# Kernel optimization log

Hardware: AMD Instinct MI355X
Metric: run time of the kernel (lower is better)

## Reference

```python
import jax, jax.numpy as jnp
import numpy as np

B, N, E, D, L, NC = 64, 128, 1024, 256, 2, 7
BETA = 0.3  # args.diffloss
BIG = 1e30  # mask_logic constant (score - (1-adj)*1e30), as in torch source lineage


def setup_inputs():
    key = jax.random.key(0)
    ks = iter(jax.random.split(key, 48))
    def p(shape, s=0.02):
        return jax.random.normal(next(ks), shape, jnp.float32) * s
    inp = {}
    inp["features"] = jax.random.normal(next(ks), (B, N, E), jnp.float32)
    inp["adj_1"] = jax.random.randint(next(ks), (B, N, N), 0, 2, jnp.int32)
    inp["adj_2"] = jax.random.randint(next(ks), (B, N, N), 0, 2, jnp.int32)
    inp["s_mask"] = jax.random.randint(next(ks), (B, N, N), 0, 2, jnp.int32)
    inp["s_mask_onehot"] = jnp.zeros((B, N, N, 2), jnp.int32)
    inp["lengths"] = jnp.full((B,), N, jnp.int32)
    inp["fc1_w"] = p((D, E)); inp["fc1_b"] = jnp.zeros((D,), jnp.float32)
    # GRUCell params (torch layout: weight_ih (3D,D) order r,z,n)
    for nm in ["gcs", "gps", "gcl", "gpl"]:
        inp[nm + "_wih"] = p((L, 3 * D, D)); inp[nm + "_whh"] = p((L, 3 * D, D))
        inp[nm + "_bih"] = jnp.zeros((L, 3 * D), jnp.float32)
        inp[nm + "_bhh"] = jnp.zeros((L, 3 * D), jnp.float32)
    # GatDot params per layer: linear1 (Q proj), linear2 (K proj)
    for nm in ["gats", "gatl"]:
        inp[nm + "_wq"] = p((L, D, D)); inp[nm + "_bq"] = jnp.zeros((L, D), jnp.float32)
        inp[nm + "_wk"] = p((L, D, D)); inp[nm + "_bk"] = jnp.zeros((L, D), jnp.float32)
    inp["affine1"] = p((2 * D, 2 * D), 0.05)
    inp["affine2"] = p((2 * D, 2 * D), 0.05)
    IN = 4 * D + E  # hidden*2*2 + emb_dim
    inp["mlp_w1"] = p((D, IN)); inp["mlp_b1"] = jnp.zeros((D,), jnp.float32)
    inp["mlp_w2"] = p((D, D)); inp["mlp_b2"] = jnp.zeros((D,), jnp.float32)
    inp["out_w"] = p((NC, D)); inp["out_b"] = jnp.zeros((NC,), jnp.float32)
    return inp


def gru_cell(x, h, wih, whh, bih, bhh):
    gi = x @ wih.T + bih
    gh = h @ whh.T + bhh
    ir, iz, in_ = jnp.split(gi, 3, axis=-1)
    hr, hz, hn = jnp.split(gh, 3, axis=-1)
    r = jax.nn.sigmoid(ir + hr)
    z = jax.nn.sigmoid(iz + hz)
    n = jnp.tanh(in_ + r * hn)
    return (1.0 - z) * n + z * h


def dag_pass(H_in, adj, gat, cpar, ppar):
    """Sequential DAG pass: per-utterance masked dot-product gather + GRU-C/GRU-P."""
    wq, bq, wk, bk = gat
    n = H_in.shape[1]
    idx = jnp.arange(n)

    def step(carry, inp):
        H1, Kb = carry            # H1: [B,N,D] written prefix; Kb = linear2(H1)
        i, x, arow = inp          # x: [B,D], arow: [B,N]
        q = x @ wq.T + bq
        scores = jnp.einsum('bnd,bd->bn', Kb, q)
        # torch: alpha - (1-adj)*1e30 over prefix :i; positions >= i excluded
        logits = scores - (1.0 - arow) * BIG - (idx >= i).astype(scores.dtype) * (2.0 * BIG)
        w = jax.nn.softmax(logits, axis=-1)
        M = jnp.einsum('bn,bnd->bd', w, H1)  # exactly 0 at i==0 (buffer zeros)
        C = gru_cell(x, M, *cpar)   # grus_c(input=x, hidden=M)
        P = gru_cell(M, x, *ppar)   # grus_p(input=M, hidden=x)
        h = C + P
        H1 = jax.lax.dynamic_update_slice(H1, h[:, None, :], (0, i, 0))
        Kb = jax.lax.dynamic_update_slice(Kb, (h @ wk.T + bk)[:, None, :], (0, i, 0))
        return (H1, Kb), None

    init = (jnp.zeros_like(H_in), jnp.zeros_like(H_in))
    xs = (idx, jnp.swapaxes(H_in, 0, 1), jnp.swapaxes(adj, 0, 1))
    (H1, _), _ = jax.lax.scan(step, init, xs)
    return H1


def diff_loss_fn(a, b):
    # orthogonality (DSN-style) loss between short/long channel features
    x = a.reshape(-1, a.shape[-1])
    y = b.reshape(-1, b.shape[-1])
    x = x - x.mean(axis=0, keepdims=True)
    y = y - y.mean(axis=0, keepdims=True)
    x = x / (jnp.linalg.norm(x, axis=1, keepdims=True) + 1e-6)
    y = y / (jnp.linalg.norm(y, axis=1, keepdims=True) + 1e-6)
    return jnp.mean((x.T @ y) ** 2)


def _forward(features, adj_1, adj_2,
             fc1_w, fc1_b,
             gcs_wih, gcs_whh, gcs_bih, gcs_bhh,
             gps_wih, gps_whh, gps_bih, gps_bhh,
             gcl_wih, gcl_whh, gcl_bih, gcl_bhh,
             gpl_wih, gpl_whh, gpl_bih, gpl_bhh,
             gats_wq, gats_bq, gats_wk, gats_bk,
             gatl_wq, gatl_bq, gatl_wk, gatl_bk,
             affine1, affine2,
             mlp_w1, mlp_b1, mlp_w2, mlp_b2, out_w, out_b):
    adj1 = adj_1.astype(jnp.float32)
    adj2 = adj_2.astype(jnp.float32)
    H0 = jax.nn.relu(features @ fc1_w.T + fc1_b)
    H0r = jax.nn.relu(features[:, ::-1] @ fc1_w.T + fc1_b)
    adj1r = adj1[:, ::-1, ::-1]
    adj2r = adj2[:, ::-1, ::-1]

    def channel(adjf, adjb, wq, bq, wk, bk, cwih, cwhh, cbih, cbhh, pwih, pwhh, pbih, pbhh):
        Hf, Hb = H0, H0r
        outs = []
        for l in range(L):
            gat = (wq[l], bq[l], wk[l], bk[l])
            cp = (cwih[l], cwhh[l], cbih[l], cbhh[l])
            pp = (pwih[l], pwhh[l], pbih[l], pbhh[l])
            Hf = dag_pass(Hf, adjf, gat, cp, pp)
            Hb = dag_pass(Hb, adjb, gat, cp, pp)
            outs.append(jnp.concatenate([Hf, Hb], axis=-1))  # no flip-back (as in source)
        return outs

    cs = channel(adj1, adj1r, gats_wq, gats_bq, gats_wk, gats_bk,
                 gcs_wih, gcs_whh, gcs_bih, gcs_bhh, gps_wih, gps_whh, gps_bih, gps_bhh)
    cl = channel(adj2, adj2r, gatl_wq, gatl_bq, gatl_wk, gatl_bk,
                 gcl_wih, gcl_whh, gcl_bih, gcl_bhh, gpl_wih, gpl_whh, gpl_bih, gpl_bhh)

    dloss = sum(diff_loss_fn(a, b) for a, b in zip(cs, cl)) * BETA

    HS, HL = cs[-1], cl[-1]  # [B,N,2D]
    A1 = jax.nn.softmax(jnp.einsum('bnd,de,bme->bnm', HS, affine1, HL), axis=-1)
    A2 = jax.nn.softmax(jnp.einsum('bnd,de,bme->bnm', HL, affine2, HS), axis=-1)
    HSn = jnp.einsum('bnm,bmd->bnd', A1, HL)
    HLn = jnp.einsum('bnm,bmd->bnd', A2, HS)

    Hfin = jnp.concatenate([features, HSn, HLn], axis=-1)  # in_dim = emb + 4D
    h = jax.nn.relu(Hfin @ mlp_w1.T + mlp_b1)
    h = jax.nn.relu(h @ mlp_w2.T + mlp_b2)
    logits = h @ out_w.T + out_b
    return logits, dloss


def reference(features, adj_1, adj_2, s_mask, s_mask_onehot, lengths,
              fc1_w, fc1_b,
              gcs_wih, gcs_whh, gcs_bih, gcs_bhh,
              gps_wih, gps_whh, gps_bih, gps_bhh,
              gcl_wih, gcl_whh, gcl_bih, gcl_bhh,
              gpl_wih, gpl_whh, gpl_bih, gpl_bhh,
              gats_wq, gats_bq, gats_wk, gats_bk,
              gatl_wq, gatl_bq, gatl_wk, gatl_bk,
              affine1, affine2,
              mlp_w1, mlp_b1, mlp_w2, mlp_b2, out_w, out_b):
    # s_mask / s_mask_onehot / lengths unused for attn_type='dotprod', no_rel_attn=True, nodal_att_type=None
    return _forward(features, adj_1, adj_2,
                    fc1_w, fc1_b,
                    gcs_wih, gcs_whh, gcs_bih, gcs_bhh,
                    gps_wih, gps_whh, gps_bih, gps_bhh,
                    gcl_wih, gcl_whh, gcl_bih, gcl_bhh,
                    gpl_wih, gpl_whh, gpl_bih, gpl_bhh,
                    gats_wq, gats_bq, gats_wk, gats_bk,
                    gatl_wq, gatl_bq, gatl_wk, gatl_bk,
                    affine1, affine2,
                    mlp_w1, mlp_b1, mlp_w2, mlp_b2, out_w, out_b)
```

## Files before the change

### kernel.cpp

```cpp
#include <hip/hip_runtime.h>
#include <hip/hip_fp16.h>
#include <math.h>

#define SB   64
#define SN   128
#define SE   1024
#define SD   256
#define SD2  512
#define SD3  768
#define SIN  2048
#define SNC  7
#define SBN  8192
#define CS   16

#define L_HS   0
#define L_GK   65536
#define L_XH   114688
#define L_QH   122880
#define L_ADJ  131072
#define L_MH   139264
#define L_LGP  139776
#define L_MP   141824
#define L_WGT  143872
#define L_PBUF 144384
#define L_S0   145408
#define SMEM_BYTES 145472

typedef _Float16 h2v __attribute__((ext_vector_type(2)));

__device__ __forceinline__ float wsum(float v){
#pragma unroll
  for (int o = 32; o; o >>= 1) v += __shfl_xor(v, o);
  return v;
}
__device__ __forceinline__ float sigm(float x){ return 1.f/(1.f + expf(-x)); }

__device__ __forceinline__ unsigned short f2h(float f){
  return __half_as_ushort(__float2half_rn(f));
}
__device__ __forceinline__ float h2f_(unsigned short u){
  return __half2float(__ushort_as_half(u));
}
__device__ __forceinline__ h2v u2h(unsigned u){
  union { unsigned u; h2v h; } c; c.u = u; return c.h;
}
__device__ __forceinline__ float dot8d(uint4 w, uint4 m, float acc){
  acc = __builtin_amdgcn_fdot2(u2h(w.x), u2h(m.x), acc, false);
  acc = __builtin_amdgcn_fdot2(u2h(w.y), u2h(m.y), acc, false);
  acc = __builtin_amdgcn_fdot2(u2h(w.z), u2h(m.z), acc, false);
  acc = __builtin_amdgcn_fdot2(u2h(w.w), u2h(m.w), acc, false);
  return acc;
}

template<bool BKMAJ, bool BIAS, bool RELU, bool ACC>
__global__ __launch_bounds__(256)
void gemm_k(const float* __restrict__ A, const float* __restrict__ Bm,
            const float* __restrict__ bias, float* __restrict__ C,
            int Nn, int K, int lda, int ldb, int ldc,
            long sA, long sB, long sC)
{
  __shared__ float As[16][132];
  __shared__ float Bs[16][68];
  const int t  = threadIdx.x;
  const int tx = t & 15, ty = t >> 4;
  const float* Ab = A + (long)blockIdx.z * sA;
  const float* Bb = Bm + (long)blockIdx.z * sB;
  float* Cb = C + (long)blockIdx.z * sC;
  const int m0 = blockIdx.y * 128, n0 = blockIdx.x * 64;
  float acc[8][4];
#pragma unroll
  for (int i = 0; i < 8; ++i)
#pragma unroll
    for (int j = 0; j < 4; ++j) acc[i][j] = 0.f;

  const int am = t >> 1, ak = (t & 1) * 8;
  int bn_ = 0, bk_ = 0;
  if (BKMAJ) { bk_ = t >> 4; bn_ = (t & 15) * 4; }
  else       { bn_ = t >> 2; bk_ = (t & 3) * 4; }

  for (int k0 = 0; k0 < K; k0 += 16) {
    const float4 a0 = *(const float4*)(Ab + (long)(m0 + am) * lda + k0 + ak);
    const float4 a1 = *(const float4*)(Ab + (long)(m0 + am) * lda + k0 + ak + 4);
    float4 b0;
    if (BKMAJ) b0 = *(const float4*)(Bb + (long)(k0 + bk_) * ldb + n0 + bn_);
    else       b0 = *(const float4*)(Bb + (long)(n0 + bn_) * ldb + k0 + bk_);
    __syncthreads();
    As[ak+0][am] = a0.x; As[ak+1][am] = a0.y; As[ak+2][am] = a0.z; As[ak+3][am] = a0.w;
    As[ak+4][am] = a1.x; As[ak+5][am] = a1.y; As[ak+6][am] = a1.z; As[ak+7][am] = a1.w;
    if (BKMAJ) { *(float4*)&Bs[bk_][bn_] = b0; }
    else { Bs[bk_+0][bn_] = b0.x; Bs[bk_+1][bn_] = b0.y; Bs[bk_+2][bn_] = b0.z; Bs[bk_+3][bn_] = b0.w; }
    __syncthreads();
#pragma unroll
    for (int kk = 0; kk < 16; ++kk) {
      float av[8], bv[4];
      *(float4*)&av[0] = *(const float4*)&As[kk][ty*8];
      *(float4*)&av[4] = *(const float4*)&As[kk][ty*8+4];
      *(float4*)&bv[0] = *(const float4*)&Bs[kk][tx*4];
#pragma unroll
      for (int ii = 0; ii < 8; ++ii)
#pragma unroll
        for (int jj = 0; jj < 4; ++jj)
          acc[ii][jj] = fmaf(av[ii], bv[jj], acc[ii][jj]);
    }
  }
#pragma unroll
  for (int ii = 0; ii < 8; ++ii) {
#pragma unroll
    for (int jj = 0; jj < 4; ++jj) {
      float v = acc[ii][jj];
      if (BIAS) v += bias[n0 + tx*4 + jj];
      const long ci = (long)(m0 + ty*8 + ii) * ldc + n0 + tx*4 + jj;
      if (ACC) v += Cb[ci];
      if (RELU) v = fmaxf(v, 0.f);
      Cb[ci] = v;
    }
  }
}

__global__ void spread_k(const float* __restrict__ src, float* __restrict__ xf,
                         float* __restrict__ xr)
{
  const int r = blockIdx.x, t = threadIdx.x;
  const int b = r >> 7, n = r & 127;
  const float v = src[(long)r * SD + t];
  xf[((long)(n * 64 + b)) * SD + t] = v;
  xr[((long)((127 - n) * 64 + b)) * SD + t] = v;
}

struct PTArgs { const float* wc[4]; const float* wp[4]; unsigned short* Wt; };
__global__ void packT_k(PTArgs a)
{
  const int kb8 = blockIdx.x, cd = blockIdx.y, t = threadIdx.x;
#pragma unroll
  for (int p = 0; p < 6; ++p) {
    const int r = t + 256 * p;
    const float* src = (r < 768) ? (a.wc[cd] + (long)r * SD)
                                 : (a.wp[cd] + (long)(r - 768) * SD);
    const float4 v0 = *(const float4*)(src + kb8 * 8);
    const float4 v1 = *(const float4*)(src + kb8 * 8 + 4);
    uint4 o;
    o.x = (unsigned)f2h(v0.x) | ((unsigned)f2h(v0.y) << 16);
    o.y = (unsigned)f2h(v0.z) | ((unsigned)f2h(v0.w) << 16);
    o.z = (unsigned)f2h(v1.x) | ((unsigned)f2h(v1.y) << 16);
    o.w = (unsigned)f2h(v1.z) | ((unsigned)f2h(v1.w) << 16);
    *(uint4*)(a.Wt + (((size_t)cd * 32 + kb8) * 1536 + r) * 8) = o;
  }
}

__global__ void s0_k(const float* __restrict__ Q, const float* __restrict__ bk,
                     float* __restrict__ S0)
{
  const int r = blockIdx.x * 4 + (threadIdx.x >> 6), lane = threadIdx.x & 63;
  const float4 q  = *(const float4*)(Q + (long)r * SD + lane * 4);
  const float4 kb = *(const float4*)(bk + lane * 4);
  float p = q.x*kb.x + q.y*kb.y + q.z*kb.z + q.w*kb.w;
  p = wsum(p);
  if (lane == 0) S0[r] = p;
}

struct StepArgs {
  const float* Qt[4]; const float* S0[4];
  const int* adj[4]; int rev[4];
  const float* bc[4];  const float* bp[4];
  const float* bgc[4]; const float* bgp[4];
  const float* X[4];
  float* H1[4];
  unsigned short* Hh;
  const unsigned short* Wt;
  const unsigned short* Wgk;
  int ldX, s0;
};
__global__ __launch_bounds__(512, 1) void step_chunk_k(StepArgs a)
{
  extern __shared__ __align__(16) char dsm[];
  unsigned short* Hs  = (unsigned short*)(dsm + L_HS);
  unsigned short* GKh = (unsigned short*)(dsm + L_GK);
  unsigned short* Xh  = (unsigned short*)(dsm + L_XH);
  unsigned short* Qh  = (unsigned short*)(dsm + L_QH);
  float* adjc = (float*)(dsm + L_ADJ);
  unsigned short* Mh  = (unsigned short*)(dsm + L_MH);
  float* lgp  = (float*)(dsm + L_LGP);
  float* Mp   = (float*)(dsm + L_MP);
  float* wgt  = (float*)(dsm + L_WGT);
  float* pbuf = (float*)(dsm + L_PBUF);
  float* s0s  = (float*)(dsm + L_S0);

  const int blk = blockIdx.x;
  const int cd = blk & 3, b = blk >> 2;
  const int t = threadIdx.x;
  const int half = t >> 8, j = t & 255;
  const int ldX = a.ldX, c0 = a.s0;
  const float* Xp  = a.X[cd];
  float* H1 = a.H1[cd];
  unsigned short* Hg = a.Hh + ((size_t)(cd * 64 + b)) * 128 * 256;
  const float* Qtp = a.Qt[cd];
  const float* S0p = a.S0[cd];
  const int*   adjp = a.adj[cd];
  const int    rev  = a.rev[cd];

  float eb0, eb1, eb2, gb0, gb1, gb2;
  if (half == 0) {
    eb0 = a.bc[cd][j];  eb1 = a.bc[cd][256+j];  eb2 = a.bc[cd][512+j];
    gb0 = a.bgc[cd][j]; gb1 = a.bgc[cd][256+j]; gb2 = a.bgc[cd][512+j];
  } else {
    eb0 = a.bp[cd][j];  eb1 = a.bp[cd][256+j];  eb2 = a.bp[cd][512+j];
    gb0 = a.bgp[cd][j]; gb1 = a.bgp[cd][256+j]; gb2 = a.bgp[cd][512+j];
  }
  const unsigned short* wb   = a.Wt  + ((size_t)cd*32*1536 + half*768 + j)*8;
  const unsigned short* wbgk = a.Wgk + ((size_t)cd*32*1536 + half*768 + j)*8;

  for (int z = t; z < CS*256; z += 512) {
    const int s = z >> 8, c = z & 255;
    Xh[z] = f2h(Xp[((long)(c0+s)*64 + b)*ldX + c]);
    Qh[z] = f2h(Qtp[((long)(c0+s)*64 + b)*SD + c]);
  }
  for (int z = t; z < CS*128; z += 512) {
    const int s = z >> 7, n = z & 127;
    const int i = c0 + s;
    int av = 0;
    if (i > 0) {
      const int ii = rev ? (SN-1-i) : i;
      const int nn = rev ? (SN-1-n) : n;
      av = adjp[((long)b*SN + ii)*SN + nn];
    }
    adjc[z] = (float)av;
  }
  if (t < CS) s0s[t] = S0p[(c0+t)*64 + b];
  for (int o = t*16; o < c0*512; o += 8192) {
    const uint4 v = *(const uint4*)((const char*)Hg + o);
    const int row = o >> 9, d2 = o & 511;
    *(uint4*)((char*)Hs + row*512 + (d2 ^ ((row & 31) << 4))) = v;
  }
  __syncthreads();

  {
    float gacc[3][CS];
#pragma unroll
    for (int g = 0; g < 3; ++g)
#pragma unroll
      for (int s = 0; s < CS; ++s) gacc[g][s] = 0.f;
    for (int kb8 = 0; kb8 < 32; ++kb8) {
      const uint4* wr = (const uint4*)(wbgk + (size_t)kb8*12288);
      const uint4 w0 = wr[0], w1 = wr[256], w2 = wr[512];
#pragma unroll
      for (int s = 0; s < CS; ++s) {
        const uint4 x8 = *(const uint4*)&Xh[s*256 + kb8*8];
        gacc[0][s] = dot8d(w0, x8, gacc[0][s]);
        gacc[1][s] = dot8d(w1, x8, gacc[1][s]);
        gacc[2][s] = dot8d(w2, x8, gacc[2][s]);
      }
    }
    const float gb[3] = {gb0, gb1, gb2};
#pragma unroll
    for (int g = 0; g < 3; ++g)
#pragma unroll
      for (int s = 0; s < CS; ++s)
        GKh[s*1536 + (half*3 + g)*256 + j] = f2h(gacc[g][s] + gb[g]);
  }
  __syncthreads();

  for (int s = 0; s < CS; ++s) {
    const int i = c0 + s;
    const float xj = Xp[((long)i*64 + b)*ldX + j];
    float mreg = 0.f;
    if (i == 0) {
      if (t < 256) Mh[t] = 0;
      __syncthreads();
    } else {
      {
        const int n = t & 127, q4 = t >> 7;
        if (n < i) {
          const char* hrow = (const char*)Hs + n*512;
          const int cx = (n & 31) << 4;
          const unsigned short* qrow = Qh + s*256 + q4*64;
          float acc = 0.f;
#pragma unroll
          for (int k = 0; k < 8; ++k) {
            const uint4 hv = *(const uint4*)(hrow + (((q4*8 + k)*16) ^ cx));
            const uint4 qv = *(const uint4*)(qrow + k*8);
            acc = dot8d(hv, qv, acc);
          }
          lgp[t] = acc;
        }
      }
      __syncthreads();
      if (t < 64) {
        const float s0v = s0s[s];
        const int l = t;
        const float lg0 = (lgp[l]      + lgp[128 + l]) + (lgp[256 + l] + lgp[384 + l]);
        const float lg1 = (lgp[64 + l] + lgp[192 + l]) + (lgp[320 + l] + lgp[448 + l]);
        const float v0 = (l < i)    ? (lg0 + s0v - (1.f - adjc[s*128+l]   )*1e30f) : -3.0e38f;
        const float v1 = (l+64 < i) ? (lg1 + s0v - (1.f - adjc[s*128+l+64])*1e30f) : -3.0e38f;
        float mx = fmaxf(v0, v1);
#pragma unroll
        for (int o = 32; o; o >>= 1) mx = fmaxf(mx, __shfl_xor(mx, o));
        const float e0 = (l < i)    ? expf(v0 - mx) : 0.f;
        const float e1 = (l+64 < i) ? expf(v1 - mx) : 0.f;
        float sum = e0 + e1;
#pragma unroll
        for (int o = 32; o; o >>= 1) sum += __shfl_xor(sum, o);
        const float inv = 1.f / sum;
        if (l < i)    wgt[l]    = e0 * inv;
        if (l+64 < i) wgt[l+64] = e1 * inv;
      }
      __syncthreads();
      {
        float m0 = 0.f, m1 = 0.f, m2 = 0.f, m3 = 0.f;
        int n = half;
        for (; n + 6 < i; n += 8) {
          m0 = fmaf(wgt[n],   h2f_(Hs[(n  )*256 + (j ^ (((n  )&31)<<3))]), m0);
          m1 = fmaf(wgt[n+2], h2f_(Hs[(n+2)*256 + (j ^ (((n+2)&31)<<3))]), m1);
          m2 = fmaf(wgt[n+4], h2f_(Hs[(n+4)*256 + (j ^ (((n+4)&31)<<3))]), m2);
          m3 = fmaf(wgt[n+6], h2f_(Hs[(n+6)*256 + (j ^ (((n+6)&31)<<3))]), m3);
        }
        for (; n < i; n += 2)
          m0 = fmaf(wgt[n], h2f_(Hs[n*256 + (j ^ ((n&31)<<3))]), m0);
        Mp[t] = (m0 + m1) + (m2 + m3);
      }
      __syncthreads();
      if (half == 0) {
        mreg = Mp[j] + Mp[256 + j];
        Mh[j] = f2h(mreg);
      }
      __syncthreads();
    }

    float g0 = 0.f, g1 = 0.f, g2 = 0.f;
    {
      const uint4* wr0 = (const uint4*)wb;
      uint4 c0r = wr0[0], c1r = wr0[256], c2r = wr0[512];
#pragma unroll 4
      for (int kb8 = 0; kb8 < 32; ++kb8) {
        uint4 n0 = c0r, n1 = c1r, n2 = c2r;
        if (kb8 < 31) {
          const uint4* wn = (const uint4*)(wb + (size_t)(kb8+1)*12288);
          n0 = wn[0]; n1 = wn[256]; n2 = wn[512];
        }
        const uint4 m8 = *(const uint4*)&Mh[kb8*8];
        g0 = dot8d(c0r, m8, g0);
        g1 = dot8d(c1r, m8, g1);
        g2 = dot8d(c2r, m8, g2);
        c0r = n0; c1r = n1; c2r = n2;
      }
    }

    {
      const int sb = s*1536;
      if (half == 1) {
        const float ghp_r = h2f_(GKh[sb + 768 + j]);
        const float ghp_z = h2f_(GKh[sb + 1024 + j]);
        const float ghp_n = h2f_(GKh[sb + 1280 + j]);
        const float rP = sigm(g0 + eb0 + ghp_r);
        const float zP = sigm(g1 + eb1 + ghp_z);
        const float nP = tanhf(g2 + eb2 + rP * ghp_n);
        pbuf[j] = (1.f - zP) * nP + zP * xj;
      }
      __syncthreads();
      if (half == 0) {
        const float gic_r = h2f_(GKh[sb + j]);
        const float gic_z = h2f_(GKh[sb + 256 + j]);
        const float gic_n = h2f_(GKh[sb + 512 + j]);
        const float rC = sigm(gic_r + g0 + eb0);
        const float zC = sigm(gic_z + g1 + eb1);
        const float nC = tanhf(gic_n + rC * (g2 + eb2));
        const float hval = (1.f - zC) * nC + zC * mreg + pbuf[j];
        H1[((long)i*64 + b)*SD2 + j] = hval;
        const unsigned short hh = f2h(hval);
        Hs[i*256 + (j ^ ((i & 31) << 3))] = hh;
        Hg[(size_t)i*256 + j] = hh;
      }
      __syncthreads();
    }
  }
}

__global__ void zero_k(float* p, long n)
{
  for (long idx = (long)blockIdx.x * 256 + threadIdx.x; idx < n; idx += (long)gridDim.x * 256)
    p[idx] = 0.f;
}

__global__ void colmean_k(const float* __restrict__ X, float* __restrict__ mean)
{
  __shared__ float red[256];
  const int c = blockIdx.x * 64 + (threadIdx.x & 63), rq = threadIdx.x >> 6;
  const int r0 = blockIdx.y * 256;
  float acc = 0.f;
  for (int r = r0 + rq; r < r0 + 256; r += 4) acc += X[(long)r * SD2 + c];
  red[threadIdx.x] = acc;
  __syncthreads();
  if (threadIdx.x < 64) {
    const float s = red[threadIdx.x] + red[64 + threadIdx.x] + red[128 + threadIdx.x] + red[192 + threadIdx.x];
    atomicAdd(&mean[c], s * (1.f / 8192.f));
  }
}

__global__ void rownorm_k(const float* __restrict__ X, const float* __restrict__ mean,
                          float* __restrict__ inv)
{
  const int r = blockIdx.x * 4 + (threadIdx.x >> 6), lane = threadIdx.x & 63;
  const float* xp = X + (long)r * SD2 + lane * 8;
  const float4 v0 = *(const float4*)xp;
  const float4 v1 = *(const float4*)(xp + 4);
  const float4 m0 = *(const float4*)(mean + lane * 8);
  const float4 m1 = *(const float4*)(mean + lane * 8 + 4);
  float ss = 0.f, d;
  d = v0.x - m0.x; ss += d*d;  d = v0.y - m0.y; ss += d*d;
  d = v0.z - m0.z; ss += d*d;  d = v0.w - m0.w; ss += d*d;
  d = v1.x - m1.x; ss += d*d;  d = v1.y - m1.y; ss += d*d;
  d = v1.z - m1.z; ss += d*d;  d = v1.w - m1.w; ss += d*d;
  ss = wsum(ss);
  if (lane == 0) inv[r] = 1.f / (sqrtf(ss) + 1e-6f);
}

__global__ __launch_bounds__(256)
void gpart_k(const float* __restrict__ X, const float* __restrict__ Y,
             const float* __restrict__ mx, const float* __restrict__ my,
             const float* __restrict__ ix, const float* __restrict__ iy,
             float* __restrict__ G)
{
  __shared__ float As[16][68];
  __shared__ float Bs[16][68];
  __shared__ float mxs[64], mys[64];
  const int t = threadIdx.x, tx = t & 15, ty = t >> 4;
  const int ci = blockIdx.y * 64, cj = blockIdx.x * 64;
  if (t < 64) { mxs[t] = mx[ci + t]; mys[t] = my[cj + t]; }
  float acc[4][4];
#pragma unroll
  for (int ii = 0; ii < 4; ++ii)
#pragma unroll
    for (int jj = 0; jj < 4; ++jj) acc[ii][jj] = 0.f;
  const int rl = t >> 4, c4 = (t & 15) * 4;
  __syncthreads();
  const int kend = blockIdx.z * 512 + 512;
  for (int kb = blockIdx.z * 512; kb < kend; kb += 16) {
    const int r = kb + rl;
    const float4 xv = *(const float4*)(X + (long)r * SD2 + ci + c4);
    const float4 yv = *(const float4*)(Y + (long)r * SD2 + cj + c4);
    const float vx = ix[r], vy = iy[r];
    __syncthreads();
    As[rl][c4+0] = (xv.x - mxs[c4+0]) * vx; As[rl][c4+1] = (xv.y - mxs[c4+1]) * vx;
    As[rl][c4+2] = (xv.z - mxs[c4+2]) * vx; As[rl][c4+3] = (xv.w - mxs[c4+3]) * vx;
    Bs[rl][c4+0] = (yv.x - mys[c4+0]) * vy; Bs[rl][c4+1] = (yv.y - mys[c4+1]) * vy;
    Bs[rl][c4+2] = (yv.z - mys[c4+2]) * vy; Bs[rl][c4+3] = (yv.w - mys[c4+3]) * vy;
    __syncthreads();
#pragma unroll
    for (int kk = 0; kk < 16; ++kk) {
      float av[4], bv[4];
      *(float4*)&av[0] = *(const float4*)&As[kk][ty*4];
      *(float4*)&bv[0] = *(const float4*)&Bs[kk][tx*4];
#pragma unroll
      for (int ii = 0; ii < 4; ++ii)
#pragma unroll
        for (int jj = 0; jj < 4; ++jj)
          acc[ii][jj] = fmaf(av[ii], bv[jj], acc[ii][jj]);
    }
  }
#pragma unroll
  for (int ii = 0; ii < 4; ++ii)
#pragma unroll
    for (int jj = 0; jj < 4; ++jj)
      atomicAdd(&G[(long)(ci + ty*4 + ii) * SD2 + cj + tx*4 + jj], acc[ii][jj]);
}

__global__ void sqsum_k(const float* __restrict__ G, float* __restrict__ dl)
{
  __shared__ float red[4];
  float s = 0.f;
  const long base = (long)blockIdx.x * 1024;
#pragma unroll
  for (int it = 0; it < 4; ++it) { const float v = G[base + it*256 + threadIdx.x]; s += v*v; }
  s = wsum(s);
  const int lane = threadIdx.x & 63, wv = threadIdx.x >> 6;
  if (lane == 0) red[wv] = s;
  __syncthreads();
  if (threadIdx.x == 0) atomicAdd(dl, red[0] + red[1] + red[2] + red[3]);
}

__global__ void smax_k(float* __restrict__ S)
{
  const int r = blockIdx.x * 4 + (threadIdx.x >> 6), lane = threadIdx.x & 63;
  float* p = S + (long)r * SN;
  const float v0 = p[lane], v1 = p[lane + 64];
  float mx = fmaxf(v0, v1);
#pragma unroll
  for (int o = 32; o; o >>= 1) mx = fmaxf(mx, __shfl_xor(mx, o));
  const float e0 = expf(v0 - mx), e1 = expf(v1 - mx);
  float s = e0 + e1;
#pragma unroll
  for (int o = 32; o; o >>= 1) s += __shfl_xor(s, o);
  const float inv = 1.f / s;
  p[lane] = e0 * inv; p[lane + 64] = e1 * inv;
}

__global__ void head_k(const float* __restrict__ H, const float* __restrict__ W,
                       const float* __restrict__ bo, float* __restrict__ out)
{
  const int r = blockIdx.x * 4 + (threadIdx.x >> 6), lane = threadIdx.x & 63;
  const float4 h = *(const float4*)(H + (long)r * SD + lane * 4);
#pragma unroll
  for (int c = 0; c < SNC; ++c) {
    const float4 w = *(const float4*)(W + (long)c * SD + lane * 4);
    float p = h.x*w.x + h.y*w.y + h.z*w.z + h.w*w.w;
    p = wsum(p);
    if (lane == 0) out[(long)r * SNC + c] = p + bo[c];
  }
}

__global__ void fin_k(const float* __restrict__ dl, float* __restrict__ out)
{
  out[0] = (dl[0] + dl[1]) * (0.3f / (512.f * 512.f));
}

extern "C" void kernel_launch(void* const* d_in, const int* in_sizes, int n_in,
                              void* d_out, int out_size, void* d_ws, size_t ws_size,
                              hipStream_t stream)
{
  (void)in_sizes; (void)n_in; (void)out_size; (void)ws_size;

  static bool attr_set = false;
  if (!attr_set) {
    hipFuncSetAttribute(reinterpret_cast<const void*>(step_chunk_k),
                        hipFuncAttributeMaxDynamicSharedMemorySize, SMEM_BYTES);
    attr_set = true;
  }

  const float* F    = (const float*)d_in[0];
  const int*   adj1 = (const int*)  d_in[1];
  const int*   adj2 = (const int*)  d_in[2];
  const float* fc1w = (const float*)d_in[6];
  const float* fc1b = (const float*)d_in[7];
  const float *g_wih[4], *g_whh[4], *g_bih[4], *g_bhh[4];
  for (int g = 0; g < 4; ++g) {
    g_wih[g] = (const float*)d_in[8 + g*4 + 0];
    g_whh[g] = (const float*)d_in[8 + g*4 + 1];
    g_bih[g] = (const float*)d_in[8 + g*4 + 2];
    g_bhh[g] = (const float*)d_in[8 + g*4 + 3];
  }
  const float* gat_wq[2] = {(const float*)d_in[24], (const float*)d_in[28]};
  const float* gat_bq[2] = {(const float*)d_in[25], (const float*)d_in[29]};
  const float* gat_wk[2] = {(const float*)d_in[26], (const float*)d_in[30]};
  const float* gat_bk[2] = {(const float*)d_in[27], (const float*)d_in[31]};
  const float* aff1 = (const float*)d_in[32];
  const float* aff2 = (const float*)d_in[33];
  const float* mw1  = (const float*)d_in[34];
  const float* mb1  = (const float*)d_in[35];
  const float* mw2  = (const float*)d_in[36];
  const float* mb2  = (const float*)d_in[37];
  const float* ow   = (const float*)d_in[38];
  const float* ob   = (const float*)d_in[39];
  float* out = (float*)d_out;

  float* ws = (float*)d_ws;
  size_t off = 0;
  auto take = [&](size_t nf){ float* p = ws + off; off += nf; return p; };
  float* region = take(22552576);
  float* X0f  = region;
  float* X0r  = region + 2097152;
  float* Qtb  = region + 4194304;
  float* Qtmp = region + 12582912;
  float* Htmp = region + 14680064;
  float* T  = region;
  float* Sb = region + 4194304;
  float* HH = region + 5242880;
  float* h1 = region + 9437184;
  float* h2 = region + 11534336;
  float* Ocat[2][2];
  for (int c = 0; c < 2; ++c) for (int l = 0; l < 2; ++l) Ocat[c][l] = take(4194304);
  float* S0b   = take(32768);
  unsigned short* WtB  = (unsigned short*)take(786432);
  unsigned short* WgkB = (unsigned short*)take(786432);
  unsigned short* HhB  = (unsigned short*)take(4194304);
  float* meanx = take(512);
  float* meany = take(512);
  float* invx  = take(8192);
  float* invy  = take(8192);
  float* dl    = take(8);
  float* Gbuf  = take(262144);

  gemm_k<false,true,true,false><<<dim3(4,64,1),256,0,stream>>>(
      F, fc1w, fc1b, Htmp, SD, SE, SE, SE, SD, 0,0,0);
  spread_k<<<SBN,256,0,stream>>>(Htmp, X0f, X0r);

  for (int l = 0; l < 2; ++l) {
    PTArgs pt, pg; StepArgs sta;
    sta.ldX = l ? SD2 : SD;
    sta.Wt = WtB; sta.Wgk = WgkB; sta.Hh = HhB;
    const int ldX = sta.ldX;
    for (int cd = 0; cd < 4; ++cd) {
      const int ch = cd >> 1;
      const float* X = (l == 0) ? ((cd & 1) ? X0r : X0f)
                                : (Ocat[ch][0] + (cd & 1) * SD);
      const float* wq   = gat_wq[ch] + l * SD * SD;
      const float* bq   = gat_bq[ch] + l * SD;
      const float* wk   = gat_wk[ch] + l * SD * SD;
      const float* bk   = gat_bk[ch] + l * SD;
      const float* cwih = g_wih[ch*2+0] + l * SD3 * SD;
      const float* cwhh = g_whh[ch*2+0] + l * SD3 * SD;
      const float* cbih = g_bih[ch*2+0] + l * SD3;
      const float* cbhh = g_bhh[ch*2+0] + l * SD3;
      const float* pwih = g_wih[ch*2+1] + l * SD3 * SD;
      const float* pwhh = g_whh[ch*2+1] + l * SD3 * SD;
      const float* pbih = g_bih[ch*2+1] + l * SD3;
      const float* pbhh = g_bhh[ch*2+1] + l * SD3;
      pt.wc[cd] = cwhh; pt.wp[cd] = pwih;
      pg.wc[cd] = cwih; pg.wp[cd] = pwhh;
      gemm_k<false,true,false,false><<<dim3(4,64,1),256,0,stream>>>(
          X, wq, bq, Qtmp, SD, SD, ldX, SD, SD, 0,0,0);
      gemm_k<true,false,false,false><<<dim3(4,64,1),256,0,stream>>>(
          Qtmp, wk, nullptr, Qtb + (size_t)cd*2097152, SD, SD, SD, SD, SD, 0,0,0);
      s0_k<<<SBN/4,256,0,stream>>>(Qtmp, bk, S0b + cd*SBN);
      float* H1mut = Ocat[ch][l] + (cd & 1) * SD;
      sta.Qt[cd] = Qtb + (size_t)cd*2097152;
      sta.S0[cd] = S0b + cd*SBN;
      sta.H1[cd] = H1mut;
      sta.adj[cd] = ch ? adj2 : adj1; sta.rev[cd] = cd & 1;
      sta.bc[cd]  = cbhh; sta.bp[cd]  = pbih;
      sta.bgc[cd] = cbih; sta.bgp[cd] = pbhh;
      sta.X[cd] = X;
    }
    pt.Wt = WtB;  packT_k<<<dim3(32,4),256,0,stream>>>(pt);
    pg.Wt = WgkB; packT_k<<<dim3(32,4),256,0,stream>>>(pg);

    for (int s0 = 0; s0 < SN; s0 += CS) {
      sta.s0 = s0;
      step_chunk_k<<<256,512,SMEM_BYTES,stream>>>(sta);
    }
  }

  zero_k<<<1,256,0,stream>>>(dl, 2);
  for (int l = 0; l < 2; ++l) {
    zero_k<<<4,256,0,stream>>>(meanx, 1024);
    colmean_k<<<dim3(8,32,1),256,0,stream>>>(Ocat[0][l], meanx);
    colmean_k<<<dim3(8,32,1),256,0,stream>>>(Ocat[1][l], meany);
    rownorm_k<<<SBN/4,256,0,stream>>>(Ocat[0][l], meanx, invx);
    rownorm_k<<<SBN/4,256,0,stream>>>(Ocat[1][l], meany, invy);
    zero_k<<<256,256,0,stream>>>(Gbuf, (long)SD2*SD2);
    gpart_k<<<dim3(8,8,16),256,0,stream>>>(Ocat[0][l], Ocat[1][l], meanx, meany, invx, invy, Gbuf);
    sqsum_k<<<256,256,0,stream>>>(Gbuf, dl + l);
  }

  gemm_k<true,false,false,false><<<dim3(8,64,1),256,0,stream>>>(
      Ocat[0][1], aff1, nullptr, T, SD2, SD2, SD2, SD2, SD2, 0,0,0);
  gemm_k<false,false,false,false><<<dim3(2,1,64),256,0,stream>>>(
      T, Ocat[1][1], nullptr, Sb, SN, SD2, 64*SD2, 64*SD2, SN, SD2, SD2, (long)SN*SN);
  smax_k<<<SBN/4,256,0,stream>>>(Sb);
  gemm_k<true,false,false,false><<<dim3(8,1,64),256,0,stream>>>(
      Sb, Ocat[1][1], nullptr, HH, SD2, SN, SN, 64*SD2, SD2, (long)SN*SN, SD2, (long)SN*SD2);
  gemm_k<false,true,false,false><<<dim3(4,64,1),256,0,stream>>>(
      F, mw1, mb1, h1, SD, SE, SE, SIN, SD, 0,0,0);
  gemm_k<false,false,false,true><<<dim3(4,64,1),256,0,stream>>>(
      HH, mw1 + 1024, nullptr, h1, SD, SD2, SD2, SIN, SD, 0,0,0);
  gemm_k<true,false,false,false><<<dim3(8,64,1),256,0,stream>>>(
      Ocat[1][1], aff2, nullptr, T, SD2, SD2, SD2, SD2, SD2, 0,0,0);
  gemm_k<false,false,false,false><<<dim3(2,1,64),256,0,stream>>>(
      T, Ocat[0][1], nullptr, Sb, SN, SD2, 64*SD2, 64*SD2, SN, SD2, SD2, (long)SN*SN);
  smax_k<<<SBN/4,256,0,stream>>>(Sb);
  gemm_k<true,false,false,false><<<dim3(8,1,64),256,0,stream>>>(
      Sb, Ocat[0][1], nullptr, HH, SD2, SN, SN, 64*SD2, SD2, (long)SN*SN, SD2, (long)SN*SD2);
  gemm_k<false,false,true,true><<<dim3(4,64,1),256,0,stream>>>(
      HH, mw1 + 1536, nullptr, h1, SD, SD2, SD2, SIN, SD, 0,0,0);
  gemm_k<false,true,true,false><<<dim3(4,64,1),256,0,stream>>>(
      h1, mw2, mb2, h2, SD, SD, SD, SD, SD, 0,0,0);
  head_k<<<SBN/4,256,0,stream>>>(h2, ow, ob, out);
  fin_k<<<1,1,0,stream>>>(dl, out + SBN * SNC);
}
```

Measured before the change: 4.553 ms.

## Prefetch GRU weights before attention phase and use lightweight LDS-only barriers

The first four k-blocks of the per-step GRU weight stream are now loaded into registers at the top of each step, so their global-memory latency overlaps the attention and softmax phases. The weight loop becomes a four-deep register pipeline. __syncthreads is replaced with a raw s_barrier that waits only on LDS counters, so the barriers no longer wait for the outstanding weight loads. This raises register pressure, and the barrier relies on every cross-thread dependency going through LDS; global writes such as H1/Hg are not fenced by it.

After: 5.314 ms. +16.7%, slower.

```diff
diff --git a/kernel.cpp b/kernel.cpp
--- a/kernel.cpp
+++ b/kernel.cpp
@@ -25,6 +25,12 @@
 #define L_PBUF 144384
 #define L_S0   145408
 #define SMEM_BYTES 145472
+
+#define RAWBAR() do { \
+  __builtin_amdgcn_sched_barrier(0); \
+  asm volatile("s_waitcnt lgkmcnt(0)" ::: "memory"); \
+  asm volatile("s_barrier" ::: "memory"); \
+  __builtin_amdgcn_sched_barrier(0); } while (0)
 
 typedef _Float16 h2v __attribute__((ext_vector_type(2)));
 
@@ -262,10 +268,24 @@
   for (int s = 0; s < CS; ++s) {
     const int i = c0 + s;
     const float xj = Xp[((long)i*64 + b)*ldX + j];
+
+    uint4 wA[3], wB[3], wC[3], wD[3];
+    {
+      const uint4* p0 = (const uint4*)wb;
+      const uint4* p1 = (const uint4*)(wb + 12288);
+      const uint4* p2 = (const uint4*)(wb + 24576);
+      const uint4* p3 = (const uint4*)(wb + 36864);
+#pragma unroll
+      for (int g = 0; g < 3; ++g) {
+        wA[g] = p0[g*256]; wB[g] = p1[g*256];
+        wC[g] = p2[g*256]; wD[g] = p3[g*256];
+      }
+    }
+
     float mreg = 0.f;
     if (i == 0) {
       if (t < 256) Mh[t] = 0;
-      __syncthreads();
+      RAWBAR();
     } else {
       {
         const int n = t & 127, q4 = t >> 7;
@@ -283,7 +303,7 @@
           lgp[t] = acc;
         }
       }
-      __syncthreads();
+      RAWBAR();
       if (t < 64) {
         const float s0v = s0s[s];
         const int l = t;
@@ -303,7 +323,7 @@
         if (l < i)    wgt[l]    = e0 * inv;
         if (l+64 < i) wgt[l+64] = e1 * inv;
       }
-      __syncthreads();
+      RAWBAR();
       {
         float m0 = 0.f, m1 = 0.f, m2 = 0.f, m3 = 0.f;
         int n = half;
@@ -317,30 +337,47 @@
           m0 = fmaf(wgt[n], h2f_(Hs[n*256 + (j ^ ((n&31)<<3))]), m0);
         Mp[t] = (m0 + m1) + (m2 + m3);
       }
-      __syncthreads();
+      RAWBAR();
       if (half == 0) {
         mreg = Mp[j] + Mp[256 + j];
         Mh[j] = f2h(mreg);
       }
-      __syncthreads();
+      RAWBAR();
     }
 
     float g0 = 0.f, g1 = 0.f, g2 = 0.f;
-    {
-      const uint4* wr0 = (const uint4*)wb;
-      uint4 c0r = wr0[0], c1r = wr0[256], c2r = wr0[512];
-#pragma unroll 4
-      for (int kb8 = 0; kb8 < 32; ++kb8) {
-        uint4 n0 = c0r, n1 = c1r, n2 = c2r;
-        if (kb8 < 31) {
-          const uint4* wn = (const uint4*)(wb + (size_t)(kb8+1)*12288);
-          n0 = wn[0]; n1 = wn[256]; n2 = wn[512];
+    for (int kb = 0; kb < 32; kb += 4) {
+      {
+        const uint4 m8 = *(const uint4*)&Mh[kb*8];
+        g0 = dot8d(wA[0], m8, g0); g1 = dot8d(wA[1], m8, g1); g2 = dot8d(wA[2], m8, g2);
+        if (kb + 4 < 32) {
+          const uint4* w = (const uint4*)(wb + (size_t)(kb+4)*12288);
+          wA[0] = w[0]; wA[1] = w[256]; wA[2] = w[512];
         }
-        const uint4 m8 = *(const uint4*)&Mh[kb8*8];
-        g0 = dot8d(c0r, m8, g0);
-        g1 = dot8d(c1r, m8, g1);
-        g2 = dot8d(c2r, m8, g2);
-        c0r = n0; c1r = n1; c2r = n2;
+      }
+      {
+        const uint4 m8 = *(const uint4*)&Mh[kb*8 + 8];
+        g0 = dot8d(wB[0], m8, g0); g1 = dot8d(wB[1], m8, g1); g2 = dot8d(wB[2], m8, g2);
+        if (kb + 5 < 32) {
+          const uint4* w = (const uint4*)(wb + (size_t)(kb+5)*12288);
+          wB[0] = w[0]; wB[1] = w[256]; wB[2] = w[512];
+        }
+      }
+      {
+        const uint4 m8 = *(const uint4*)&Mh[kb*8 + 16];
+        g0 = dot8d(wC[0], m8, g0); g1 = dot8d(wC[1], m8, g1); g2 = dot8d(wC[2], m8, g2);
+        if (kb + 6 < 32) {
+          const uint4* w = (const uint4*)(wb + (size_t)(kb+6)*12288);
+          wC[0] = w[0]; wC[1] = w[256]; wC[2] = w[512];
+        }
+      }
+      {
+        const uint4 m8 = *(const uint4*)&Mh[kb*8 + 24];
+        g0 = dot8d(wD[0], m8, g0); g1 = dot8d(wD[1], m8, g1); g2 = dot8d(wD[2], m8, g2);
+        if (kb + 7 < 32) {
+          const uint4* w = (const uint4*)(wb + (size_t)(kb+7)*12288);
+          wD[0] = w[0]; wD[1] = w[256]; wD[2] = w[512];
+        }
       }
     }
 
@@ -355,7 +392,7 @@
         const float nP = tanhf(g2 + eb2 + rP * ghp_n);
         pbuf[j] = (1.f - zP) * nP + zP * xj;
       }
-      __syncthreads();
+      RAWBAR();
       if (half == 0) {
         const float gic_r = h2f_(GKh[sb + j]);
         const float gic_z = h2f_(GKh[sb + 256 + j]);
@@ -369,7 +406,7 @@
         Hs[i*256 + (j ^ ((i & 31) << 3))] = hh;
         Hg[(size_t)i*256 + j] = hh;
       }
-      __syncthreads();
+      RAWBAR();
     }
   }
 }
```
